# Kernel tuning notes

Measured on AMD Instinct MI355X. Metric: run time of the kernel, lower is better.

Reference implementation:

```python
import jax, jax.numpy as jnp
import numpy as np

D_MODEL = 1024
NUM_HEADS = 16
D_K = D_MODEL // NUM_HEADS
D_FF = 4096
EPS = 1e-5


def _layernorm(x, gamma, beta):
    mu = jnp.mean(x, axis=-1, keepdims=True)
    var = jnp.mean(jnp.square(x - mu), axis=-1, keepdims=True)
    return (x - mu) * jax.lax.rsqrt(var + EPS) * gamma + beta


def setup_inputs() -> dict:
    key = jax.random.key(0)
    ks = jax.random.split(key, 16)
    B, S = 4, 2048
    s_in = 1.0 / np.sqrt(D_MODEL)
    s_ff = 1.0 / np.sqrt(D_FF)
    inp = {
        "x": jax.random.normal(ks[0], (B, S, D_MODEL), jnp.float32),
        "src_mask": jnp.ones((B, 1, 1, S), jnp.int32),
        "w_q": jax.random.normal(ks[1], (D_MODEL, D_MODEL), jnp.float32) * s_in,
        "b_q": jnp.zeros((D_MODEL,), jnp.float32),
        "w_k": jax.random.normal(ks[2], (D_MODEL, D_MODEL), jnp.float32) * s_in,
        "b_k": jnp.zeros((D_MODEL,), jnp.float32),
        "w_v": jax.random.normal(ks[3], (D_MODEL, D_MODEL), jnp.float32) * s_in,
        "b_v": jnp.zeros((D_MODEL,), jnp.float32),
        "w_o": jax.random.normal(ks[4], (D_MODEL, D_MODEL), jnp.float32) * s_in,
        "b_o": jnp.zeros((D_MODEL,), jnp.float32),
        "w1": jax.random.normal(ks[5], (D_MODEL, D_FF), jnp.float32) * s_in,
        "b1": jnp.zeros((D_FF,), jnp.float32),
        "w2": jax.random.normal(ks[6], (D_FF, D_MODEL), jnp.float32) * s_ff,
        "b2": jnp.zeros((D_MODEL,), jnp.float32),
        "g1": jnp.ones((D_MODEL,), jnp.float32),
        "be1": jnp.zeros((D_MODEL,), jnp.float32),
        "g2": jnp.ones((D_MODEL,), jnp.float32),
        "be2": jnp.zeros((D_MODEL,), jnp.float32),
    }
    return inp


def reference(x, src_mask, w_q, b_q, w_k, b_k, w_v, b_v, w_o, b_o,
              w1, b1, w2, b2, g1, be1, g2, be2):
    B, S, _ = x.shape

    def split_heads(t):  # [B,S,D] -> [B,H,S,dk]
        return t.reshape(B, S, NUM_HEADS, D_K).transpose(0, 2, 1, 3)

    q = split_heads(x @ w_q + b_q)
    k = split_heads(x @ w_k + b_k)
    v = split_heads(x @ w_v + b_v)

    scores = jnp.einsum("bhqd,bhkd->bhqk", q, k) / np.sqrt(D_K)
    scores = jnp.where(src_mask == 0, -jnp.inf, scores)
    attn = jax.nn.softmax(scores, axis=-1)
    ctx = jnp.einsum("bhqk,bhkd->bhqd", attn, v)
    merged = ctx.transpose(0, 2, 1, 3).reshape(B, S, D_MODEL)
    attn_out = merged @ w_o + b_o

    h = _layernorm(x + attn_out, g1, be1)
    ff = jax.nn.relu(h @ w1 + b1) @ w2 + b2
    return _layernorm(h + ff, g2, be2)
```

## Files before the change

kernel.cpp:

```cpp
#include <hip/hip_runtime.h>

typedef unsigned short u16;
typedef __attribute__((ext_vector_type(4))) unsigned short u16x4;
typedef __attribute__((ext_vector_type(8))) short bf16x8;
typedef __attribute__((ext_vector_type(4))) float f32x4;

__device__ inline float bf2f(u16 u) {
  union { unsigned int i; float f; } v; v.i = ((unsigned int)u) << 16; return v.f;
}
__device__ inline u16 f2bf(float f) {
  union { float f; unsigned int i; } v; v.f = f;
  unsigned int r = v.i + 0x7fffu + ((v.i >> 16) & 1u);
  return (u16)(r >> 16);
}
__device__ inline unsigned int pack2bf(float lo, float hi) {
  union { float f; unsigned int i; } a, b; a.f = lo; b.f = hi;
  return __builtin_amdgcn_perm(b.i + 0x8000u, a.i + 0x8000u, 0x07060302u);
}

typedef const __attribute__((address_space(1))) unsigned int* gas_t;
typedef __attribute__((address_space(3))) unsigned int* las_t;
__device__ inline void gload_lds16(const u16* g, u16* l) {
  __builtin_amdgcn_global_load_lds((gas_t)(unsigned long long)(const void*)g,
                                   (las_t)(unsigned int)(unsigned long long)(void*)l,
                                   16, 0, 0);
}

__global__ __launch_bounds__(256) void cvt_bf16(const float* __restrict__ src,
                                                u16* __restrict__ dst, int n) {
  int i = (blockIdx.x * 256 + threadIdx.x) * 4;
  if (i >= n) return;
  float4 v = *(const float4*)(src + i);
  u16x4 o;
  o.x = f2bf(v.x); o.y = f2bf(v.y); o.z = f2bf(v.z); o.w = f2bf(v.w);
  *(u16x4*)(dst + i) = o;
}

__global__ __launch_bounds__(256) void concat3(const float* __restrict__ a,
                                               const float* __restrict__ b,
                                               const float* __restrict__ c,
                                               float* __restrict__ o, int n) {
  int i = blockIdx.x * 256 + threadIdx.x;
  if (i >= n) return;
  o[i] = a[i]; o[n + i] = b[i]; o[2 * n + i] = c[i];
}

__global__ __launch_bounds__(256) void transpose_f32_bf16(const float* __restrict__ src,
                                                          u16* __restrict__ dst,
                                                          int R, int C) {
  __shared__ u16 tile[32][33];
  int tx = threadIdx.x & 31, ty = threadIdx.x >> 5;
  int c0 = blockIdx.x * 32, r0 = blockIdx.y * 32;
  #pragma unroll
  for (int i = ty; i < 32; i += 8)
    tile[i][tx] = f2bf(src[(size_t)(r0 + i) * C + c0 + tx]);
  __syncthreads();
  #pragma unroll
  for (int i = ty; i < 32; i += 8)
    dst[(size_t)(c0 + i) * R + r0 + tx] = tile[tx][i];
}

__global__ __launch_bounds__(256) void transpose_v(const u16* __restrict__ src,
                                                   u16* __restrict__ VT,
                                                   int B, int S, int H, int RS, int CO) {
  __shared__ u16 tile[32][33];
  int tx = threadIdx.x & 31, ty = threadIdx.x >> 5;
  int s0 = blockIdx.x * 32, d0 = blockIdx.y * 32;
  int bh = blockIdx.z;
  int b = bh / H, h = bh % H;
  #pragma unroll
  for (int i = ty; i < 32; i += 8)
    tile[i][tx] = src[(size_t)(b * S + s0 + i) * RS + CO + h * 64 + d0 + tx];
  __syncthreads();
  #pragma unroll
  for (int i = ty; i < 32; i += 8)
    VT[((size_t)bh * 64 + d0 + i) * S + s0 + tx] = tile[tx][i];
}

__global__ __launch_bounds__(256) void gemm_bt(const u16* __restrict__ A,
                                               const u16* __restrict__ Bt,
                                               const float* __restrict__ bias,
                                               u16* __restrict__ C,
                                               int M, int N, int K, int relu) {
  __shared__ u16 As[128 * 32];
  __shared__ u16 Bs[128 * 32];
  const int tid = threadIdx.x;
  const int lane = tid & 63, wid = tid >> 6;
  const int lr = lane & 15, quad = lane >> 4;
  const int wm = (wid >> 1) * 64, wn = (wid & 1) * 64;
  const int m0 = blockIdx.y * 128, n0 = blockIdx.x * 128;
  const int lrow = lane >> 2;
  const int lcol = (lane & 3) * 8;

  f32x4 acc[4][4];
  const f32x4 zero = {0.f, 0.f, 0.f, 0.f};
  #pragma unroll
  for (int mt = 0; mt < 4; ++mt)
    #pragma unroll
    for (int nt = 0; nt < 4; ++nt) acc[mt][nt] = zero;

  for (int k0 = 0; k0 < K; k0 += 32) {
    #pragma unroll
    for (int it = 0; it < 2; ++it) {
      int rbase = wid * 32 + it * 16;
      gload_lds16(A + (size_t)(m0 + rbase + lrow) * K + k0 + lcol, &As[rbase * 32]);
      gload_lds16(Bt + (size_t)(n0 + rbase + lrow) * K + k0 + lcol, &Bs[rbase * 32]);
    }
    __syncthreads();
    bf16x8 af[4], bfr[4];
    #pragma unroll
    for (int mt = 0; mt < 4; ++mt)
      af[mt] = *(const bf16x8*)(&As[(wm + mt * 16 + lr) * 32 + quad * 8]);
    #pragma unroll
    for (int nt = 0; nt < 4; ++nt)
      bfr[nt] = *(const bf16x8*)(&Bs[(wn + nt * 16 + lr) * 32 + quad * 8]);
    #pragma unroll
    for (int mt = 0; mt < 4; ++mt)
      #pragma unroll
      for (int nt = 0; nt < 4; ++nt)
        acc[mt][nt] = __builtin_amdgcn_mfma_f32_16x16x32_bf16(af[mt], bfr[nt], acc[mt][nt], 0, 0, 0);
    __syncthreads();
  }

  #pragma unroll
  for (int nt = 0; nt < 4; ++nt) {
    int n = n0 + wn + nt * 16 + lr;
    float bv = bias[n];
    #pragma unroll
    for (int mt = 0; mt < 4; ++mt) {
      #pragma unroll
      for (int i = 0; i < 4; ++i) {
        int m = m0 + wm + mt * 16 + quad * 4 + i;
        float v = acc[mt][nt][i] + bv;
        if (relu) v = fmaxf(v, 0.f);
        C[(size_t)m * N + n] = f2bf(v);
      }
    }
  }
}

__global__ __launch_bounds__(256) void flash_attn(const u16* __restrict__ Qp,
                                                  const u16* __restrict__ Kp,
                                                  const u16* __restrict__ VT,
                                                  const int* __restrict__ mask,
                                                  u16* __restrict__ ctx,
                                                  int B, int S, int H, int QSTR) {
  __shared__ u16 kt_lds[64 * 72];
  __shared__ u16 vt_lds[64 * 72];
  __shared__ u16 p_lds[4 * 16 * 72];
  __shared__ float msk_lds[64];
  const int tid = threadIdx.x;
  const int lane = tid & 63, wid = tid >> 6;
  const int lr = lane & 15, quad = lane >> 4;
  const int bh = blockIdx.y;
  const int b = bh / H, h = bh % H;
  const int q0 = blockIdx.x * 64;
  const u16* vt_base = VT + (size_t)bh * 64 * S;
  const float SC = 0.125f * 1.44269504089f;

  bf16x8 qf[2];
  {
    int qm = q0 + wid * 16 + lr;
    const u16* qptr = Qp + (size_t)(b * S + qm) * QSTR + h * 64;
    qf[0] = *(const bf16x8*)(qptr + quad * 8);
    qf[1] = *(const bf16x8*)(qptr + 32 + quad * 8);
  }

  float m_i = -1e30f, l_i = 0.f;
  float O[4][4];
  #pragma unroll
  for (int nt = 0; nt < 4; ++nt)
    #pragma unroll
    for (int i = 0; i < 4; ++i) O[nt][i] = 0.f;

  u16* pw = &p_lds[wid * 16 * 72];

  for (int kt = 0; kt < S; kt += 64) {
    #pragma unroll
    for (int it = 0; it < 2; ++it) {
      int c = tid + it * 256;
      int r = c >> 3;
      int cc = (c & 7) * 8;
      uint4 kv = *(const uint4*)(Kp + (size_t)(b * S + kt + r) * QSTR + h * 64 + cc);
      *(uint4*)(&kt_lds[r * 72 + cc]) = kv;
      uint4 vv = *(const uint4*)(vt_base + (size_t)r * S + kt + cc);
      *(uint4*)(&vt_lds[r * 72 + cc]) = vv;
    }
    if (tid < 64) msk_lds[tid] = mask[b * S + kt + tid] ? 0.f : -1e30f;
    __syncthreads();

    float s[4][4];
    #pragma unroll
    for (int st = 0; st < 4; ++st) {
      f32x4 c = {0.f, 0.f, 0.f, 0.f};
      bf16x8 kf0 = *(const bf16x8*)(&kt_lds[(st * 16 + lr) * 72 + quad * 8]);
      bf16x8 kf1 = *(const bf16x8*)(&kt_lds[(st * 16 + lr) * 72 + 32 + quad * 8]);
      c = __builtin_amdgcn_mfma_f32_16x16x32_bf16(kf0, qf[0], c, 0, 0, 0);
      c = __builtin_amdgcn_mfma_f32_16x16x32_bf16(kf1, qf[1], c, 0, 0, 0);
      float4 mv = *(const float4*)(&msk_lds[st * 16 + quad * 4]);
      s[st][0] = c[0] * SC + mv.x;
      s[st][1] = c[1] * SC + mv.y;
      s[st][2] = c[2] * SC + mv.z;
      s[st][3] = c[3] * SC + mv.w;
    }

    float tmax = s[0][0];
    #pragma unroll
    for (int st = 0; st < 4; ++st)
      #pragma unroll
      for (int i = 0; i < 4; ++i) tmax = fmaxf(tmax, s[st][i]);
    tmax = fmaxf(tmax, __shfl_xor(tmax, 16, 64));
    tmax = fmaxf(tmax, __shfl_xor(tmax, 32, 64));
    float mn = fmaxf(m_i, tmax);
    float al = exp2f(m_i - mn);
    m_i = mn;
    float rs = 0.f;
    #pragma unroll
    for (int st = 0; st < 4; ++st)
      #pragma unroll
      for (int i = 0; i < 4; ++i) {
        float p = exp2f(s[st][i] - mn);
        s[st][i] = p; rs += p;
      }
    rs += __shfl_xor(rs, 16, 64);
    rs += __shfl_xor(rs, 32, 64);
    l_i = l_i * al + rs;

    #pragma unroll
    for (int st = 0; st < 4; ++st) {
      uint2 pk;
      pk.x = pack2bf(s[st][0], s[st][1]);
      pk.y = pack2bf(s[st][2], s[st][3]);
      *(uint2*)(&pw[lr * 72 + st * 16 + quad * 4]) = pk;
    }

    bf16x8 pf0 = *(const bf16x8*)(&pw[lr * 72 + quad * 8]);
    bf16x8 pf1 = *(const bf16x8*)(&pw[lr * 72 + 32 + quad * 8]);
    #pragma unroll
    for (int nt = 0; nt < 4; ++nt) {
      f32x4 c;
      c[0] = O[nt][0] * al; c[1] = O[nt][1] * al;
      c[2] = O[nt][2] * al; c[3] = O[nt][3] * al;
      bf16x8 vf0 = *(const bf16x8*)(&vt_lds[(nt * 16 + lr) * 72 + quad * 8]);
      bf16x8 vf1 = *(const bf16x8*)(&vt_lds[(nt * 16 + lr) * 72 + 32 + quad * 8]);
      c = __builtin_amdgcn_mfma_f32_16x16x32_bf16(vf0, pf0, c, 0, 0, 0);
      c = __builtin_amdgcn_mfma_f32_16x16x32_bf16(vf1, pf1, c, 0, 0, 0);
      O[nt][0] = c[0]; O[nt][1] = c[1]; O[nt][2] = c[2]; O[nt][3] = c[3];
    }
    __syncthreads();
  }

  float linv = 1.f / fmaxf(l_i, 1e-30f);
  int q = q0 + wid * 16 + lr;
  u16* op = ctx + (size_t)(b * S + q) * (H * 64) + h * 64;
  #pragma unroll
  for (int nt = 0; nt < 4; ++nt) {
    u16x4 o;
    o.x = f2bf(O[nt][0] * linv); o.y = f2bf(O[nt][1] * linv);
    o.z = f2bf(O[nt][2] * linv); o.w = f2bf(O[nt][3] * linv);
    *(u16x4*)(op + nt * 16 + quad * 4) = o;
  }
}

__device__ inline float block_reduce_sum(float v, float* sbuf) {
  #pragma unroll
  for (int m = 1; m < 64; m <<= 1) v += __shfl_xor(v, m, 64);
  int w = threadIdx.x >> 6;
  if ((threadIdx.x & 63) == 0) sbuf[w] = v;
  __syncthreads();
  v = sbuf[0] + sbuf[1] + sbuf[2] + sbuf[3];
  __syncthreads();
  return v;
}

__global__ __launch_bounds__(256) void add_ln(const float* __restrict__ a32,
                                              const u16* __restrict__ a16,
                                              const u16* __restrict__ b,
                                              const float* __restrict__ g,
                                              const float* __restrict__ be,
                                              u16* __restrict__ out16,
                                              float* __restrict__ out32, int D) {
  __shared__ float sbuf[4];
  int row = blockIdx.x;
  size_t base = (size_t)row * D;
  int i = threadIdx.x * 4;
  float v[4];
  {
    u16x4 bv = *(const u16x4*)(b + base + i);
    if (a32) {
      float4 av = *(const float4*)(a32 + base + i);
      v[0] = av.x + bf2f(bv.x); v[1] = av.y + bf2f(bv.y);
      v[2] = av.z + bf2f(bv.z); v[3] = av.w + bf2f(bv.w);
    } else {
      u16x4 av = *(const u16x4*)(a16 + base + i);
      v[0] = bf2f(av.x) + bf2f(bv.x); v[1] = bf2f(av.y) + bf2f(bv.y);
      v[2] = bf2f(av.z) + bf2f(bv.z); v[3] = bf2f(av.w) + bf2f(bv.w);
    }
  }
  float sum = v[0] + v[1] + v[2] + v[3];
  sum = block_reduce_sum(sum, sbuf);
  float mean = sum / (float)D;
  float var = 0.f;
  #pragma unroll
  for (int j = 0; j < 4; ++j) { float d = v[j] - mean; var += d * d; }
  var = block_reduce_sum(var, sbuf);
  float rstd = rsqrtf(var / (float)D + 1e-5f);
  float4 gv = *(const float4*)(g + i);
  float4 bev = *(const float4*)(be + i);
  float o0 = (v[0] - mean) * rstd * gv.x + bev.x;
  float o1 = (v[1] - mean) * rstd * gv.y + bev.y;
  float o2 = (v[2] - mean) * rstd * gv.z + bev.z;
  float o3 = (v[3] - mean) * rstd * gv.w + bev.w;
  if (out32) {
    float4 o = {o0, o1, o2, o3};
    *(float4*)(out32 + base + i) = o;
  } else {
    u16x4 o;
    o.x = f2bf(o0); o.y = f2bf(o1); o.z = f2bf(o2); o.w = f2bf(o3);
    *(u16x4*)(out16 + base + i) = o;
  }
}

extern "C" void kernel_launch(void* const* d_in, const int* in_sizes, int n_in,
                              void* d_out, int out_size, void* d_ws, size_t ws_size,
                              hipStream_t stream) {
  (void)in_sizes; (void)n_in; (void)out_size; (void)ws_size;
  const float* x   = (const float*)d_in[0];
  const int* mask  = (const int*)d_in[1];
  const float* wq  = (const float*)d_in[2];
  const float* bq  = (const float*)d_in[3];
  const float* wk  = (const float*)d_in[4];
  const float* bk  = (const float*)d_in[5];
  const float* wv  = (const float*)d_in[6];
  const float* bv  = (const float*)d_in[7];
  const float* wo  = (const float*)d_in[8];
  const float* bo  = (const float*)d_in[9];
  const float* w1  = (const float*)d_in[10];
  const float* b1  = (const float*)d_in[11];
  const float* w2  = (const float*)d_in[12];
  const float* b2  = (const float*)d_in[13];
  const float* g1  = (const float*)d_in[14];
  const float* be1 = (const float*)d_in[15];
  const float* g2  = (const float*)d_in[16];
  const float* be2 = (const float*)d_in[17];

  const int B = 4, S = 2048, D = 1024, H = 16, DFF = 4096;
  const int D3 = 3 * D;
  const size_t TOK = (size_t)B * S;
  const size_t TD = TOK * D;

  u16* ws   = (u16*)d_ws;
  u16* QKVp = ws;
  u16* xb   = ws + 3 * TD;
  u16* VT   = xb;
  u16* CTX  = ws + 4 * TD;
  u16* ATT  = ws + 5 * TD;
  u16* Hb   = ws + 6 * TD;
  u16* QKVT = ws + 7 * TD;
  u16* WOT  = QKVT + 3 * (size_t)D * D;
  u16* W1T  = WOT + (size_t)D * D;
  u16* FF1  = ws;
  u16* FF2  = ATT;
  u16* W2T  = QKVT;
  float* biasc = (float*)CTX;

  dim3 blk(256);

  cvt_bf16<<<dim3((unsigned)(TD / (256 * 4))), blk, 0, stream>>>(x, xb, (int)TD);
  concat3<<<dim3(4), blk, 0, stream>>>(bq, bk, bv, biasc, D);

  transpose_f32_bf16<<<dim3(D / 32, D / 32), blk, 0, stream>>>(wq, QKVT, D, D);
  transpose_f32_bf16<<<dim3(D / 32, D / 32), blk, 0, stream>>>(wk, QKVT + (size_t)D * D, D, D);
  transpose_f32_bf16<<<dim3(D / 32, D / 32), blk, 0, stream>>>(wv, QKVT + 2 * (size_t)D * D, D, D);
  transpose_f32_bf16<<<dim3(D / 32, D / 32), blk, 0, stream>>>(wo, WOT, D, D);
  transpose_f32_bf16<<<dim3(DFF / 32, D / 32), blk, 0, stream>>>(w1, W1T, D, DFF);

  gemm_bt<<<dim3(D3 / 128, TOK / 128), blk, 0, stream>>>(xb, QKVT, biasc, QKVp, (int)TOK, D3, D, 0);

  transpose_v<<<dim3(S / 32, 2, B * H), blk, 0, stream>>>(QKVp, VT, B, S, H, D3, 2 * D);

  flash_attn<<<dim3(S / 64, B * H), blk, 0, stream>>>(QKVp, QKVp + D, VT, mask, CTX, B, S, H, D3);

  gemm_bt<<<dim3(D / 128, TOK / 128), blk, 0, stream>>>(CTX, WOT, bo, ATT, (int)TOK, D, D, 0);

  transpose_f32_bf16<<<dim3(D / 32, DFF / 32), blk, 0, stream>>>(w2, W2T, DFF, D);

  add_ln<<<dim3((unsigned)TOK), blk, 0, stream>>>(x, (const u16*)nullptr, ATT, g1, be1,
                                                  Hb, (float*)nullptr, D);

  gemm_bt<<<dim3(DFF / 128, TOK / 128), blk, 0, stream>>>(Hb, W1T, b1, FF1, (int)TOK, DFF, D, 1);
  gemm_bt<<<dim3(D / 128, TOK / 128), blk, 0, stream>>>(FF1, W2T, b2, FF2, (int)TOK, D, DFF, 0);

  add_ln<<<dim3((unsigned)TOK), blk, 0, stream>>>((const float*)nullptr, Hb, FF2, g2, be2,
                                                  (u16*)nullptr, (float*)d_out, D);
}
```

Baseline: 680.7 us.

## Load K/V tiles via global_load_lds with XOR swizzle, add lazy softmax rescale

The flash attention kernel now fills the K and V^T LDS tiles with direct global-to-LDS loads into an unpadded layout whose XOR swizzle avoids bank conflicts, instead of staging through registers. The online softmax skips rescaling unless the max grows past a threshold (8 in the exp2 domain), and the row-sum cross-lane reduction is deferred to the end. It also uses the hardware packed bf16 convert and raises wave priority around the MFMA sections. The intent is to cut register staging, VALU work and per-tile shuffles. The lazy rescale risks reduced numerical headroom if scores grow large.

```diff
diff --git a/kernel.cpp b/kernel.cpp
--- a/kernel.cpp
+++ b/kernel.cpp
@@ -13,9 +13,10 @@
   unsigned int r = v.i + 0x7fffu + ((v.i >> 16) & 1u);
   return (u16)(r >> 16);
 }
-__device__ inline unsigned int pack2bf(float lo, float hi) {
-  union { float f; unsigned int i; } a, b; a.f = lo; b.f = hi;
-  return __builtin_amdgcn_perm(b.i + 0x8000u, a.i + 0x8000u, 0x07060302u);
+__device__ inline unsigned int cvt_pk_bf16(float lo, float hi) {
+  unsigned int r;
+  asm("v_cvt_pk_bf16_f32 %0, %1, %2" : "=v"(r) : "v"(lo), "v"(hi));
+  return r;
 }
 
 typedef const __attribute__((address_space(1))) unsigned int* gas_t;
@@ -145,8 +146,8 @@
                                                   const int* __restrict__ mask,
                                                   u16* __restrict__ ctx,
                                                   int B, int S, int H, int QSTR) {
-  __shared__ u16 kt_lds[64 * 72];
-  __shared__ u16 vt_lds[64 * 72];
+  __shared__ u16 kt_lds[64 * 64];
+  __shared__ u16 vt_lds[64 * 64];
   __shared__ u16 p_lds[4 * 16 * 72];
   __shared__ float msk_lds[64];
   const int tid = threadIdx.x;
@@ -158,6 +159,10 @@
   const u16* vt_base = VT + (size_t)bh * 64 * S;
   const float SC = 0.125f * 1.44269504089f;
 
+  const int srl = lane >> 3;
+  const int scol = ((lane & 7) ^ srl) * 8;
+  const int swz = (lr & 7) << 3;
+
   bf16x8 qf[2];
   {
     int qm = q0 + wid * 16 + lr;
@@ -167,34 +172,34 @@
   }
 
   float m_i = -1e30f, l_i = 0.f;
-  float O[4][4];
-  #pragma unroll
-  for (int nt = 0; nt < 4; ++nt)
-    #pragma unroll
-    for (int i = 0; i < 4; ++i) O[nt][i] = 0.f;
+  f32x4 O[4];
+  #pragma unroll
+  for (int nt = 0; nt < 4; ++nt) {
+    O[nt][0] = 0.f; O[nt][1] = 0.f; O[nt][2] = 0.f; O[nt][3] = 0.f;
+  }
 
   u16* pw = &p_lds[wid * 16 * 72];
+  const u16* kgp = Kp + ((size_t)b * S + wid * 16 + srl) * QSTR + h * 64 + scol;
+  const u16* vgp = vt_base + (size_t)(wid * 16 + srl) * S + scol;
+  u16* klb = &kt_lds[(wid * 16) * 64];
+  u16* vlb = &vt_lds[(wid * 16) * 64];
 
   for (int kt = 0; kt < S; kt += 64) {
-    #pragma unroll
-    for (int it = 0; it < 2; ++it) {
-      int c = tid + it * 256;
-      int r = c >> 3;
-      int cc = (c & 7) * 8;
-      uint4 kv = *(const uint4*)(Kp + (size_t)(b * S + kt + r) * QSTR + h * 64 + cc);
-      *(uint4*)(&kt_lds[r * 72 + cc]) = kv;
-      uint4 vv = *(const uint4*)(vt_base + (size_t)r * S + kt + cc);
-      *(uint4*)(&vt_lds[r * 72 + cc]) = vv;
-    }
+    gload_lds16(kgp + (size_t)kt * QSTR, klb);
+    gload_lds16(kgp + (size_t)(kt + 8) * QSTR, klb + 8 * 64);
+    gload_lds16(vgp + kt, vlb);
+    gload_lds16(vgp + 8 * (size_t)S + kt, vlb + 8 * 64);
     if (tid < 64) msk_lds[tid] = mask[b * S + kt + tid] ? 0.f : -1e30f;
     __syncthreads();
 
     float s[4][4];
+    __builtin_amdgcn_s_setprio(1);
     #pragma unroll
     for (int st = 0; st < 4; ++st) {
       f32x4 c = {0.f, 0.f, 0.f, 0.f};
-      bf16x8 kf0 = *(const bf16x8*)(&kt_lds[(st * 16 + lr) * 72 + quad * 8]);
-      bf16x8 kf1 = *(const bf16x8*)(&kt_lds[(st * 16 + lr) * 72 + 32 + quad * 8]);
+      const u16* kr = &kt_lds[(st * 16 + lr) * 64];
+      bf16x8 kf0 = *(const bf16x8*)(kr + ((quad * 8) ^ swz));
+      bf16x8 kf1 = *(const bf16x8*)(kr + ((32 + quad * 8) ^ swz));
       c = __builtin_amdgcn_mfma_f32_16x16x32_bf16(kf0, qf[0], c, 0, 0, 0);
       c = __builtin_amdgcn_mfma_f32_16x16x32_bf16(kf1, qf[1], c, 0, 0, 0);
       float4 mv = *(const float4*)(&msk_lds[st * 16 + quad * 4]);
@@ -203,6 +208,7 @@
       s[st][2] = c[2] * SC + mv.z;
       s[st][3] = c[3] * SC + mv.w;
     }
+    __builtin_amdgcn_s_setprio(0);
 
     float tmax = s[0][0];
     #pragma unroll
@@ -211,45 +217,51 @@
       for (int i = 0; i < 4; ++i) tmax = fmaxf(tmax, s[st][i]);
     tmax = fmaxf(tmax, __shfl_xor(tmax, 16, 64));
     tmax = fmaxf(tmax, __shfl_xor(tmax, 32, 64));
-    float mn = fmaxf(m_i, tmax);
-    float al = exp2f(m_i - mn);
-    m_i = mn;
+    if (__any(tmax > m_i + 8.0f)) {
+      float mn = fmaxf(m_i, tmax);
+      float al = exp2f(m_i - mn);
+      m_i = mn;
+      l_i *= al;
+      #pragma unroll
+      for (int nt = 0; nt < 4; ++nt) {
+        O[nt][0] *= al; O[nt][1] *= al; O[nt][2] *= al; O[nt][3] *= al;
+      }
+    }
     float rs = 0.f;
     #pragma unroll
     for (int st = 0; st < 4; ++st)
       #pragma unroll
       for (int i = 0; i < 4; ++i) {
-        float p = exp2f(s[st][i] - mn);
+        float p = exp2f(s[st][i] - m_i);
         s[st][i] = p; rs += p;
       }
-    rs += __shfl_xor(rs, 16, 64);
-    rs += __shfl_xor(rs, 32, 64);
-    l_i = l_i * al + rs;
+    l_i += rs;
 
     #pragma unroll
     for (int st = 0; st < 4; ++st) {
       uint2 pk;
-      pk.x = pack2bf(s[st][0], s[st][1]);
-      pk.y = pack2bf(s[st][2], s[st][3]);
+      pk.x = cvt_pk_bf16(s[st][0], s[st][1]);
+      pk.y = cvt_pk_bf16(s[st][2], s[st][3]);
       *(uint2*)(&pw[lr * 72 + st * 16 + quad * 4]) = pk;
     }
 
     bf16x8 pf0 = *(const bf16x8*)(&pw[lr * 72 + quad * 8]);
     bf16x8 pf1 = *(const bf16x8*)(&pw[lr * 72 + 32 + quad * 8]);
+    __builtin_amdgcn_s_setprio(1);
     #pragma unroll
     for (int nt = 0; nt < 4; ++nt) {
-      f32x4 c;
-      c[0] = O[nt][0] * al; c[1] = O[nt][1] * al;
-      c[2] = O[nt][2] * al; c[3] = O[nt][3] * al;
-      bf16x8 vf0 = *(const bf16x8*)(&vt_lds[(nt * 16 + lr) * 72 + quad * 8]);
-      bf16x8 vf1 = *(const bf16x8*)(&vt_lds[(nt * 16 + lr) * 72 + 32 + quad * 8]);
-      c = __builtin_amdgcn_mfma_f32_16x16x32_bf16(vf0, pf0, c, 0, 0, 0);
-      c = __builtin_amdgcn_mfma_f32_16x16x32_bf16(vf1, pf1, c, 0, 0, 0);
-      O[nt][0] = c[0]; O[nt][1] = c[1]; O[nt][2] = c[2]; O[nt][3] = c[3];
-    }
+      const u16* vr = &vt_lds[(nt * 16 + lr) * 64];
+      bf16x8 vf0 = *(const bf16x8*)(vr + ((quad * 8) ^ swz));
+      bf16x8 vf1 = *(const bf16x8*)(vr + ((32 + quad * 8) ^ swz));
+      O[nt] = __builtin_amdgcn_mfma_f32_16x16x32_bf16(vf0, pf0, O[nt], 0, 0, 0);
+      O[nt] = __builtin_amdgcn_mfma_f32_16x16x32_bf16(vf1, pf1, O[nt], 0, 0, 0);
+    }
+    __builtin_amdgcn_s_setprio(0);
     __syncthreads();
   }
 
+  l_i += __shfl_xor(l_i, 16, 64);
+  l_i += __shfl_xor(l_i, 32, 64);
   float linv = 1.f / fmaxf(l_i, 1e-30f);
   int q = q0 + wid * 16 + lr;
   u16* op = ctx + (size_t)(b * S + q) * (H * 64) + h * 64;
```

New measurement: 659.0 us. -3.2%, faster.
